# Optimization experiments

Hardware: AMD Instinct MI355X
Metric: run time of the kernel (lower is better)

## Reference

```python
import jax, jax.numpy as jnp
import numpy as np

H = 512   # hidden_size
E = 512   # embedding_size
V = 32000 # vocabulary_size
B = 64    # batch
TS = 256  # source length
TD = 64   # decoder (target) length


def setup_inputs() -> dict:
    key = jax.random.key(0)
    ks = jax.random.split(key, 10)
    s = lambda k, shape, sc: (jax.random.normal(k, shape, jnp.float32) * sc)
    return dict(
        src_seq=jax.random.randint(ks[0], (B, TS), 0, V, dtype=jnp.int32),
        dec_seq=jax.random.randint(ks[1], (B, TD), 0, V, dtype=jnp.int32),
        emb=s(ks[2], (V, E), 0.02),
        enc_Wx=s(ks[3], (E, 3 * H), 1.0 / np.sqrt(E)),
        enc_Wh=s(ks[4], (H, 3 * H), 1.0 / np.sqrt(H)),
        enc_b=jnp.zeros((3 * H,), jnp.float32),
        dec_Wx=s(ks[5], (E + H, 3 * H), 1.0 / np.sqrt(E + H)),
        dec_Wh=s(ks[6], (H, 3 * H), 1.0 / np.sqrt(H)),
        dec_b=jnp.zeros((3 * H,), jnp.float32),
        W_att=s(ks[7], (H, H), 1.0 / np.sqrt(H)),
        Wd=s(ks[8], (H, V), 1.0 / np.sqrt(H)),
        bd=jnp.zeros((V,), jnp.float32),
    )


def gru_step(h, x, Wx, Wh, b):
    # Keras GRUCell math (gate order z, r, h; reset_after applied on recurrent term)
    gx = x @ Wx + b            # [B, 3H]
    rec = h @ Wh               # [B, 3H]
    z = jax.nn.sigmoid(gx[:, :H] + rec[:, :H])
    r = jax.nn.sigmoid(gx[:, H:2 * H] + rec[:, H:2 * H])
    hh = jnp.tanh(gx[:, 2 * H:] + r * rec[:, 2 * H:])
    return z * h + (1.0 - z) * hh


def reference(src_seq, dec_seq, emb, enc_Wx, enc_Wh, enc_b,
              dec_Wx, dec_Wh, dec_b, W_att, Wd, bd):
    src_e = emb[src_seq]   # [B, TS, E]
    dec_e = emb[dec_seq]   # [B, TD, E]

    # ---- encoder: GRU over source, collecting hidden state each step ----
    def enc_f(h, x):
        h2 = gru_step(h, x, enc_Wx, enc_Wh, enc_b)
        return h2, h2

    h0 = jnp.zeros((src_e.shape[0], H), src_e.dtype)
    h_last, enc_hs = jax.lax.scan(enc_f, h0, jnp.swapaxes(src_e, 0, 1))
    enc_hs = jnp.swapaxes(enc_hs, 0, 1)  # [B, TS, H]

    # ---- decoder: Luong 'general' attention + GRU step each timestep ----
    def dec_f(h, x):
        q = h @ W_att                                          # [B, H]
        attn = jax.nn.softmax(jnp.einsum('bth,bh->bt', enc_hs, q), axis=-1)
        ctx = jnp.einsum('bt,bth->bh', attn, enc_hs)           # [B, H]
        inp = jnp.concatenate([x, ctx], axis=1)                # [B, E+H]
        h2 = gru_step(h, inp, dec_Wx, dec_Wh, dec_b)
        return h2, h2

    _, outs = jax.lax.scan(dec_f, h_last, jnp.swapaxes(dec_e, 0, 1))
    outs = jnp.swapaxes(outs, 0, 1)  # [B, TD, H]

    # ---- vocab projection ----
    logits = outs @ Wd + bd          # [B, TD, V]
    return logits
```

## Files before the change

kernel.cpp:

```cpp
#include <hip/hip_runtime.h>
#include <stdint.h>
#include <math.h>

#define B_   64
#define TS_  256
#define TD_  64
#define H_   512
#define E_   512
#define V_   32000
#define G3_  1536

#define ENC_G 0
#define ENC_T 128
#define ENC_F 160
#define DH_G  192
#define DH_T  320
#define DH_F  352
#define DP_G  384
#define DP_T  512
#define DP_F  544

typedef unsigned short u16;
typedef __attribute__((ext_vector_type(8))) short  short8v;
typedef __attribute__((ext_vector_type(4))) float  float4v;

__device__ __forceinline__ u16 f2bf(float x) {
  union { float f; unsigned u; } v; v.f = x;
  unsigned r = v.u + 0x7FFFu + ((v.u >> 16) & 1u);
  return (u16)(r >> 16);
}
__device__ __forceinline__ float bf2f(u16 h) {
  union { unsigned u; float f; } v; v.u = ((unsigned)h) << 16; return v.f;
}
__device__ __forceinline__ float sigm(float x) { return 1.f / (1.f + expf(-x)); }

__device__ __forceinline__ float4v mfma16(short8v a, short8v b, float4v c) {
  return __builtin_amdgcn_mfma_f32_16x16x32_bf16(a, b, c, 0, 0, 0);
}

__device__ __forceinline__ void st2_sc(u16* p, u16 v) {
  unsigned vv = v;
  asm volatile("global_store_short %0, %1, off sc0 sc1" :: "v"(p), "v"(vv) : "memory");
}
__device__ __forceinline__ void st4_sc(float* p, float v) {
  asm volatile("global_store_dword %0, %1, off sc0 sc1" :: "v"(p), "v"(v) : "memory");
}
__device__ __forceinline__ void st4u_sc(unsigned* p, unsigned v) {
  asm volatile("global_store_dword %0, %1, off sc0 sc1" :: "v"(p), "v"(v) : "memory");
}
__device__ __forceinline__ void st8_sc(float* p, float2 v) {
  asm volatile("global_store_dwordx2 %0, %1, off sc0 sc1" :: "v"(p), "v"(v) : "memory");
}
__device__ __forceinline__ short8v ld16_sc(const u16* p) {
  short8v r;
  asm volatile("global_load_dwordx4 %0, %1, off sc0 sc1\ns_waitcnt vmcnt(0)"
               : "=v"(r) : "v"(p) : "memory");
  return r;
}
__device__ __forceinline__ unsigned ld_cnt(const unsigned* p) {
  unsigned r;
  asm volatile("global_load_dword %0, %1, off sc0 sc1\ns_waitcnt vmcnt(0)"
               : "=v"(r) : "v"(p) : "memory");
  return r;
}

__device__ __forceinline__ void block_arrive(unsigned* bars, int goff, int grp,
                                             int toff, int foff, unsigned ngrp, unsigned step) {
  asm volatile("s_waitcnt vmcnt(0)" ::: "memory");
  __syncthreads();
  if (threadIdx.x == 0) {
    unsigned o = __hip_atomic_fetch_add(bars + goff + (grp << 5), 1u,
                                        __ATOMIC_RELAXED, __HIP_MEMORY_SCOPE_AGENT);
    if (o == step * 32u - 1u) {
      unsigned o2 = __hip_atomic_fetch_add(bars + toff, 1u,
                                           __ATOMIC_RELAXED, __HIP_MEMORY_SCOPE_AGENT);
      if (o2 == step * ngrp - 1u)
        st4u_sc(bars + foff, step);
    }
  }
}
__device__ __forceinline__ void wait_flag(unsigned* bars, int foff, unsigned step, unsigned* sdead) {
  __syncthreads();
  if (threadIdx.x == 0 && !*sdead) {
    unsigned spins = 0;
    while (ld_cnt(bars + foff) < step) {
      __builtin_amdgcn_s_sleep(4);
      if (++spins > (1u << 23)) { *sdead = 1u; break; }
    }
  }
  __syncthreads();
}

__global__ __launch_bounds__(256) void k_embed(const int* __restrict__ seq,
    const float* __restrict__ emb, u16* __restrict__ hi, u16* __restrict__ lo, int total8) {
  int idx = blockIdx.x * 256 + threadIdx.x;
  if (idx >= total8) return;
  int row = idx >> 6;
  int c8  = (idx & 63) << 3;
  const float* src = emb + (size_t)seq[row] * E_ + c8;
  short8v hv, lv;
  #pragma unroll
  for (int i = 0; i < 8; ++i) {
    float x = src[i];
    u16 hb2 = f2bf(x);
    hv[i] = (short)hb2;
    lv[i] = (short)f2bf(x - bf2f(hb2));
  }
  *(short8v*)(hi + (size_t)idx * 8) = hv;
  *(short8v*)(lo + (size_t)idx * 8) = lv;
}

template<bool LO>
__global__ __launch_bounds__(256) void k_transp(const float* __restrict__ src, int ld,
    u16* __restrict__ dh, u16* __restrict__ dl, int K, int N) {
  __shared__ float t[64][65];
  int n0 = blockIdx.x << 6, k0 = blockIdx.y << 6;
  int c = threadIdx.x & 63, r0 = threadIdx.x >> 6;
  #pragma unroll
  for (int i = 0; i < 16; ++i) {
    int r = r0 + (i << 2);
    t[r][c] = src[(size_t)(k0 + r) * ld + n0 + c];
  }
  __syncthreads();
  #pragma unroll
  for (int i = 0; i < 16; ++i) {
    int rr = r0 + (i << 2);
    float v = t[c][rr];
    u16 hb2 = f2bf(v);
    size_t o = (size_t)(n0 + rr) * K + k0 + c;
    dh[o] = hb2;
    if (LO) dl[o] = f2bf(v - bf2f(hb2));
  }
}

__global__ __launch_bounds__(256) void k_cvt(const float* __restrict__ s, u16* __restrict__ d, int n) {
  int i = blockIdx.x * 256 + threadIdx.x;
  if (i < n) d[i] = f2bf(s[i]);
}

__device__ __forceinline__ int swzA(int row, int q) {
  return (row << 5) + ((q ^ ((row >> 1) & 3)) << 3);
}

template<bool SPLIT, bool BF32N, bool BIAS, bool OBF>
__global__ __launch_bounds__(256, 2) void k_gemm(
    const u16* __restrict__ Ah, const u16* __restrict__ Al,
    const u16* __restrict__ Bh, const u16* __restrict__ Bl,
    const float* __restrict__ Bf,
    float* __restrict__ C, u16* __restrict__ Cb, const float* __restrict__ bias,
    int M, int N, int K)
{
  __shared__ u16 sA[4096], sB[4096];
  __shared__ u16 sA2[SPLIT ? 4096 : 16], sB2[SPLIT ? 4096 : 16];
  const int tid = threadIdx.x;
  const int ln = tid & 63, wv = tid >> 6;
  const int wr = wv >> 1, wc = wv & 1;
  const int m0 = blockIdx.y << 7, n0 = blockIdx.x << 7;
  const int lm = ln & 15, lq = ln >> 4;
  const float4v zf = {0.f, 0.f, 0.f, 0.f};

  float4v acc[4][4];
  #pragma unroll
  for (int i = 0; i < 4; ++i)
    #pragma unroll
    for (int j = 0; j < 4; ++j) acc[i][j] = zf;

  for (int kt = 0; kt < K; kt += 32) {
    #pragma unroll
    for (int s = 0; s < 2; ++s) {
      int id = tid + (s << 8);
      int row = id >> 2, q = id & 3;
      size_t goA = (size_t)(m0 + row) * K + kt + (q << 3);
      int lo = swzA(row, q);
      *(short8v*)&sA[lo] = *(const short8v*)(Ah + goA);
      if constexpr (!BF32N) {
        size_t goB = (size_t)(n0 + row) * K + kt + (q << 3);
        *(short8v*)&sB[lo] = *(const short8v*)(Bh + goB);
        if constexpr (SPLIT) {
          *(short8v*)&sA2[lo] = *(const short8v*)(Al + goA);
          *(short8v*)&sB2[lo] = *(const short8v*)(Bl + goB);
        }
      }
    }
    if constexpr (BF32N) {
      int k = tid >> 3, nc = (tid & 7) << 4;
      const float* bp = Bf + (size_t)(kt + k) * N + n0 + nc;
      int q = k >> 3, e = k & 7;
      #pragma unroll
      for (int j = 0; j < 16; ++j)
        sB[swzA(nc + j, q) + e] = f2bf(bp[j]);
    }
    __syncthreads();
    short8v af[4], bfr[4];
    #pragma unroll
    for (int i = 0; i < 4; ++i) {
      af[i]  = *(const short8v*)&sA[swzA((wr << 6) + (i << 4) + lm, lq)];
      bfr[i] = *(const short8v*)&sB[swzA((wc << 6) + (i << 4) + lm, lq)];
    }
    if constexpr (SPLIT) {
      short8v af2[4], bfr2[4];
      #pragma unroll
      for (int i = 0; i < 4; ++i) {
        af2[i]  = *(const short8v*)&sA2[swzA((wr << 6) + (i << 4) + lm, lq)];
        bfr2[i] = *(const short8v*)&sB2[swzA((wc << 6) + (i << 4) + lm, lq)];
      }
      #pragma unroll
      for (int mi = 0; mi < 4; ++mi)
        #pragma unroll
        for (int ni = 0; ni < 4; ++ni) {
          acc[mi][ni] = mfma16(af[mi],  bfr[ni],  acc[mi][ni]);
          acc[mi][ni] = mfma16(af2[mi], bfr[ni],  acc[mi][ni]);
          acc[mi][ni] = mfma16(af[mi],  bfr2[ni], acc[mi][ni]);
        }
    } else {
      #pragma unroll
      for (int mi = 0; mi < 4; ++mi)
        #pragma unroll
        for (int ni = 0; ni < 4; ++ni)
          acc[mi][ni] = mfma16(af[mi], bfr[ni], acc[mi][ni]);
    }
    __syncthreads();
  }
  #pragma unroll
  for (int mi = 0; mi < 4; ++mi)
    #pragma unroll
    for (int ni = 0; ni < 4; ++ni) {
      int col = n0 + (wc << 6) + (ni << 4) + lm;
      float bv = BIAS ? bias[col] : 0.f;
      #pragma unroll
      for (int i = 0; i < 4; ++i) {
        int row = m0 + (wr << 6) + (mi << 4) + (lq << 2) + i;
        float v = acc[mi][ni][i] + bv;
        size_t o = (size_t)row * N + col;
        if (OBF) Cb[o] = f2bf(v);
        else     C[o] = v;
      }
    }
}

__global__ __launch_bounds__(256, 1) void k_encoder(
    const float* __restrict__ gx, const float* __restrict__ Wh,
    u16* hb, u16* __restrict__ ehs, unsigned* bars)
{
  __shared__ char smem[32768];
  __shared__ float rec_s[3][16][16];
  __shared__ unsigned sdead;
  const int tid = threadIdx.x, bid = blockIdx.x;
  const int ln = tid & 63, wv = tid >> 6;
  const int lm = ln & 15, lq = ln >> 4, lq8 = lq << 3;
  const int set = bid >> 5, colblk = bid & 31, grp = bid >> 5;
  const int s16 = set << 4;
  const int jx = tid & 15, bl = tid >> 4;
  const int jg = (colblk << 4) + jx;
  const int b  = s16 + bl;
  if (tid == 0) sdead = 0;

  short8v wfh[16], wfl[16];
  if (wv < 3) {
    const int col = (wv << 9) + (colblk << 4) + lm;
    #pragma unroll
    for (int kt = 0; kt < 16; ++kt) {
      short8v a, b2;
      #pragma unroll
      for (int i = 0; i < 8; ++i) {
        float w = Wh[(size_t)((kt << 5) + lq8 + i) * G3_ + col];
        u16 hb2 = f2bf(w);
        a[i]  = (short)hb2;
        b2[i] = (short)f2bf(w - bf2f(hb2));
      }
      wfh[kt] = a; wfl[kt] = b2;
    }
  }
  const float4v zf = {0.f, 0.f, 0.f, 0.f};
  for (int t = 0; t < TS_; ++t) {
    if (t == 0) {
      short8v zz = {0,0,0,0,0,0,0,0};
      #pragma unroll
      for (int i = 0; i < 8; ++i)
        *(short8v*)(smem + ((tid + (i << 8)) << 4)) = zz;
      __syncthreads();
    } else {
      wait_flag(bars, ENC_F, (unsigned)t, &sdead);
      const u16* cur = hb + ((t & 1) ? 65536 : 0);
      short8v v[8];
      #pragma unroll
      for (int i = 0; i < 8; ++i) {
        int c = tid + (i << 8);
        int half = c >> 10, rem = c & 1023;
        int r = rem >> 6, col16 = rem & 63;
        const u16* p = cur + (half << 15) + ((s16 + r) << 9) + (col16 << 3);
        asm volatile("global_load_dwordx4 %0, %1, off sc0 sc1" : "=v"(v[i]) : "v"(p));
      }
      asm volatile("s_waitcnt vmcnt(0)" ::: "memory");
      __builtin_amdgcn_sched_barrier(0);
      #pragma unroll
      for (int i = 0; i < 8; ++i) {
        int c = tid + (i << 8);
        int half = c >> 10, rem = c & 1023;
        int r = rem >> 6, col16 = rem & 63;
        *(short8v*)(smem + ((half << 14) | (r << 10) | ((col16 << 4) ^ ((r & 7) << 4)))) = v[i];
      }
      __syncthreads();
    }
    float gzv, grv, ghv;
    {
      size_t rg = (size_t)((b << 8) + t) * G3_ + jg;
      gzv = gx[rg]; grv = gx[rg + 512]; ghv = gx[rg + 1024];
    }
    int hoff = (bl << 10) | ((jg << 1) ^ ((bl & 7) << 4));
    float hold = bf2f(*(const u16*)(smem + hoff)) + bf2f(*(const u16*)(smem + 16384 + hoff));
    if (wv < 3) {
      float4v acc = zf;
      #pragma unroll
      for (int kt = 0; kt < 16; ++kt) {
        int aoff = (lm << 10) | (((kt << 6) + (lq << 4)) ^ ((lm & 7) << 4));
        short8v ah = *(const short8v*)(smem + aoff);
        short8v al = *(const short8v*)(smem + 16384 + aoff);
        acc = mfma16(ah, wfh[kt], acc);
        acc = mfma16(al, wfh[kt], acc);
        acc = mfma16(ah, wfl[kt], acc);
      }
      #pragma unroll
      for (int i = 0; i < 4; ++i) rec_s[wv][(lq << 2) + i][lm] = acc[i];
    }
    __syncthreads();
    {
      float z  = sigm(gzv + rec_s[0][bl][jx]);
      float r  = sigm(grv + rec_s[1][bl][jx]);
      float hh = tanhf(ghv + r * rec_s[2][bl][jx]);
      float hnew = z * hold + (1.f - z) * hh;
      u16 nh = f2bf(hnew);
      u16* hnx = hb + ((t & 1) ? 0 : 65536);
      st2_sc(hnx + (b << 9) + jg, nh);
      st2_sc(hnx + 32768 + (b << 9) + jg, f2bf(hnew - bf2f(nh)));
      ehs[(size_t)((b << 8) + t) * 512 + jg] = nh;
    }
    if (t < TS_ - 1)
      block_arrive(bars, ENC_G, grp, ENC_T, ENC_F, 4u, (unsigned)(t + 1));
  }
}

__global__ __launch_bounds__(256, 1) void k_decoder(
    const float* __restrict__ gxd, const float* __restrict__ Wh,
    const u16* __restrict__ att, const u16* __restrict__ e2,
    u16* hb, float* pnum, float* pden, u16* __restrict__ outs, unsigned* bars)
{
  __shared__ char smem[32768];
  __shared__ float rec_s[3][16][16];
  __shared__ u16 shs[2][512];
  __shared__ float ps[128][2];
  __shared__ float es[128];
  __shared__ float wsum[2];
  __shared__ unsigned sdead;
  const int tid = threadIdx.x, bid = blockIdx.x;
  const int ln = tid & 63, wv = tid >> 6;
  const int lm = ln & 15, lq = ln >> 4, lq8 = lq << 3;
  const bool isrec = (bid < 128);
  const int set = bid >> 5, colblk = bid & 31;
  const int s16 = set << 4;
  const int jx = tid & 15, bl = tid >> 4;
  const int jg = (colblk << 4) + jx;
  const int b  = s16 + bl;
  const int ab = bid - 128, batt = ab >> 1, cset = ab & 1;
  if (tid == 0) sdead = 0;
  __syncthreads();

  short8v wfh[16], wfl[16];
  if (isrec && wv < 3) {
    const int col = (wv << 9) + (colblk << 4) + lm;
    #pragma unroll
    for (int kt = 0; kt < 16; ++kt) {
      short8v a, b2;
      #pragma unroll
      for (int i = 0; i < 8; ++i) {
        float w = Wh[(size_t)((kt << 5) + lq8 + i) * G3_ + col];
        u16 hb2 = f2bf(w);
        a[i]  = (short)hb2;
        b2[i] = (short)f2bf(w - bf2f(hb2));
      }
      wfh[kt] = a; wfl[kt] = b2;
    }
  }
  const float4v zf = {0.f, 0.f, 0.f, 0.f};
  for (int t = 0; t < TD_; ++t) {
    const u16* cur = hb + ((t & 1) ? 65536 : 0);
    if (isrec) {
      if (t) wait_flag(bars, DH_F, (unsigned)t, &sdead);
      {
        short8v v[8];
        #pragma unroll
        for (int i = 0; i < 8; ++i) {
          int c = tid + (i << 8);
          int half = c >> 10, rem = c & 1023;
          int r = rem >> 6, col16 = rem & 63;
          const u16* p = cur + (half << 15) + ((s16 + r) << 9) + (col16 << 3);
          asm volatile("global_load_dwordx4 %0, %1, off sc0 sc1" : "=v"(v[i]) : "v"(p));
        }
        asm volatile("s_waitcnt vmcnt(0)" ::: "memory");
        __builtin_amdgcn_sched_barrier(0);
        #pragma unroll
        for (int i = 0; i < 8; ++i) {
          int c = tid + (i << 8);
          int half = c >> 10, rem = c & 1023;
          int r = rem >> 6, col16 = rem & 63;
          *(short8v*)(smem + ((half << 14) | (r << 10) | ((col16 << 4) ^ ((r & 7) << 4)))) = v[i];
        }
        __syncthreads();
      }
      float gzv, grv, ghv;
      {
        size_t rg = (size_t)((b << 6) + t) * G3_ + jg;
        gzv = gxd[rg]; grv = gxd[rg + 512]; ghv = gxd[rg + 1024];
      }
      int hoff = (bl << 10) | ((jg << 1) ^ ((bl & 7) << 4));
      float hold = bf2f(*(const u16*)(smem + hoff)) + bf2f(*(const u16*)(smem + 16384 + hoff));
      if (wv < 3) {
        float4v acc = zf;
        #pragma unroll
        for (int kt = 0; kt < 16; ++kt) {
          int aoff = (lm << 10) | (((kt << 6) + (lq << 4)) ^ ((lm & 7) << 4));
          short8v ah = *(const short8v*)(smem + aoff);
          short8v al = *(const short8v*)(smem + 16384 + aoff);
          acc = mfma16(ah, wfh[kt], acc);
          acc = mfma16(al, wfh[kt], acc);
          acc = mfma16(ah, wfl[kt], acc);
        }
        #pragma unroll
        for (int i = 0; i < 4; ++i) rec_s[wv][(lq << 2) + i][lm] = acc[i];
      }
      __syncthreads();
      wait_flag(bars, DP_F, (unsigned)(t + 1), &sdead);
      {
        const float* p0 = pnum + (size_t)(b << 1) * G3_ + jg;
        const float* p1 = p0 + G3_;
        float pv0, pv1, pv2, pv3, pv4, pv5, d0, d1;
        asm volatile("global_load_dword %0, %1, off sc0 sc1" : "=v"(pv0) : "v"(p0));
        asm volatile("global_load_dword %0, %1, off sc0 sc1" : "=v"(pv1) : "v"(p0 + 512));
        asm volatile("global_load_dword %0, %1, off sc0 sc1" : "=v"(pv2) : "v"(p0 + 1024));
        asm volatile("global_load_dword %0, %1, off sc0 sc1" : "=v"(pv3) : "v"(p1));
        asm volatile("global_load_dword %0, %1, off sc0 sc1" : "=v"(pv4) : "v"(p1 + 512));
        asm volatile("global_load_dword %0, %1, off sc0 sc1" : "=v"(pv5) : "v"(p1 + 1024));
        asm volatile("global_load_dword %0, %1, off sc0 sc1" : "=v"(d0) : "v"(pden + (b << 1)));
        asm volatile("global_load_dword %0, %1, off sc0 sc1" : "=v"(d1) : "v"(pden + (b << 1) + 1));
        asm volatile("s_waitcnt vmcnt(0)" ::: "memory");
        __builtin_amdgcn_sched_barrier(0);
        float inv = 1.f / (d0 + d1);
        float z  = sigm(gzv + (pv0 + pv3) * inv + rec_s[0][bl][jx]);
        float r  = sigm(grv + (pv1 + pv4) * inv + rec_s[1][bl][jx]);
        float hh = tanhf(ghv + (pv2 + pv5) * inv + r * rec_s[2][bl][jx]);
        float hnew = z * hold + (1.f - z) * hh;
        u16 nh = f2bf(hnew);
        outs[(size_t)((b << 6) + t) * 512 + jg] = nh;
        if (t < TD_ - 1) {
          u16* hnx = hb + ((t & 1) ? 0 : 65536);
          st2_sc(hnx + (b << 9) + jg, nh);
          st2_sc(hnx + 32768 + (b << 9) + jg, f2bf(hnew - bf2f(nh)));
        }
      }
      if (t < TD_ - 1)
        block_arrive(bars, DH_G, set, DH_T, DH_F, 4u, (unsigned)(t + 1));
    } else {
      if (t) wait_flag(bars, DH_F, (unsigned)t, &sdead);
      if (tid < 128) {
        int half = tid >> 6, cc = tid & 63;
        short8v hv = ld16_sc(cur + (half << 15) + (batt << 9) + (cc << 3));
        *(short8v*)&shs[half][cc << 3] = hv;
      }
      __syncthreads();
      {
        int tt = tid >> 1, kq = tid & 1;
        const u16* ep = att + (size_t)((batt << 8) + (cset << 7) + tt) * 512 + (kq << 8);
        float s = 0.f;
        #pragma unroll 4
        for (int k8 = 0; k8 < 32; ++k8) {
          short8v ev = *(const short8v*)(ep + (k8 << 3));
          short8v xh = *(const short8v*)&shs[0][(kq << 8) + (k8 << 3)];
          short8v xl = *(const short8v*)&shs[1][(kq << 8) + (k8 << 3)];
          #pragma unroll
          for (int i = 0; i < 8; ++i)
            s += bf2f((u16)ev[i]) * (bf2f((u16)xh[i]) + bf2f((u16)xl[i]));
        }
        ps[tt][kq] = s;
      }
      __syncthreads();
      if (tid < 128) {
        float e = expf(ps[tid][0] + ps[tid][1]);
        es[tid] = e;
        #pragma unroll
        for (int off = 32; off; off >>= 1) e += __shfl_down(e, off);
        if ((tid & 63) == 0) wsum[tid >> 6] = e;
      }
      __syncthreads();
      if (tid == 0) st4_sc(&pden[(batt << 1) + cset], wsum[0] + wsum[1]);
      {
        int c0 = tid * 6;
        float a0=0.f,a1=0.f,a2=0.f,a3=0.f,a4=0.f,a5=0.f;
        const u16* base = e2 + (size_t)((batt << 8) + (cset << 7)) * G3_ + c0;
        for (int tt = 0; tt < 128; ++tt) {
          float ev = es[tt];
          const u16* p = base + (size_t)tt * G3_;
          a0 += ev * bf2f(p[0]); a1 += ev * bf2f(p[1]); a2 += ev * bf2f(p[2]);
          a3 += ev * bf2f(p[3]); a4 += ev * bf2f(p[4]); a5 += ev * bf2f(p[5]);
        }
        float* pn = pnum + (size_t)((batt << 1) + cset) * G3_ + c0;
        float2 v01 = {a0, a1}, v23 = {a2, a3}, v45 = {a4, a5};
        st8_sc(pn, v01); st8_sc(pn + 2, v23); st8_sc(pn + 4, v45);
      }
      block_arrive(bars, DP_G, ab >> 5, DP_T, DP_F, 4u, (unsigned)(t + 1));
    }
  }
}

extern "C" void kernel_launch(void* const* d_in, const int* in_sizes, int n_in,
                              void* d_out, int out_size, void* d_ws, size_t ws_size,
                              hipStream_t stream) {
  const int*   src_seq = (const int*)d_in[0];
  const int*   dec_seq = (const int*)d_in[1];
  const float* emb     = (const float*)d_in[2];
  const float* enc_Wx  = (const float*)d_in[3];
  const float* enc_Wh  = (const float*)d_in[4];
  const float* enc_b   = (const float*)d_in[5];
  const float* dec_Wx  = (const float*)d_in[6];
  const float* dec_Wh  = (const float*)d_in[7];
  const float* dec_b   = (const float*)d_in[8];
  const float* W_att   = (const float*)d_in[9];
  const float* Wd      = (const float*)d_in[10];
  const float* bd      = (const float*)d_in[11];

  char* ob = (char*)d_out;
  float* gx_all  = (float*)(ob + 0);
  float* gxd_all = (float*)(ob + 100663296);
  u16* srcE_h = (u16*)(ob + 125829120);
  u16* srcE_l = (u16*)(ob + 142606336);
  u16* decE_h = (u16*)(ob + 159383552);
  u16* decE_l = (u16*)(ob + 163577856);
  u16* ehs    = (u16*)(ob + 167772160);
  u16* attb   = (u16*)(ob + 184549376);
  u16* e2b    = (u16*)(ob + 201326592);
  u16* wxT_h  = (u16*)(ob + 251658240);
  u16* wxT_l  = (u16*)(ob + 253231104);
  u16* wdxT_h = (u16*)(ob + 254803968);
  u16* wdxT_l = (u16*)(ob + 256376832);
  u16* wxcT   = (u16*)(ob + 257949696);
  u16* watt   = (u16*)(ob + 259522560);
  u16* hbuf   = (u16*)(ob + 260046848);

  char* wb = (char*)d_ws;
  u16* outs     = (u16*)(wb + 0);
  float* pnum   = (float*)(wb + 4194304);
  float* pden   = (float*)(wb + 4980736);
  unsigned* bars = (unsigned*)(wb + 4981248);
  (void)in_sizes; (void)n_in; (void)out_size; (void)ws_size;

  hipMemsetAsync(bars, 0, 4096, stream);

  k_embed<<<4096, 256, 0, stream>>>(src_seq, emb, srcE_h, srcE_l, B_*TS_*64);
  k_embed<<<1024, 256, 0, stream>>>(dec_seq, emb, decE_h, decE_l, B_*TD_*64);
  k_transp<true ><<<dim3(24, 8), 256, 0, stream>>>(enc_Wx, G3_, wxT_h,  wxT_l,  512, G3_);
  k_transp<true ><<<dim3(24, 8), 256, 0, stream>>>(dec_Wx, G3_, wdxT_h, wdxT_l, 512, G3_);
  k_transp<false><<<dim3(24, 8), 256, 0, stream>>>(dec_Wx + (size_t)512*G3_, G3_, wxcT, nullptr, 512, G3_);
  k_cvt<<<1024, 256, 0, stream>>>(W_att, watt, 512*512);

  k_gemm<true, false, true, false><<<dim3(12, 128), 256, 0, stream>>>(
      srcE_h, srcE_l, wxT_h, wxT_l, nullptr, gx_all, nullptr, enc_b, 16384, G3_, 512);
  k_gemm<true, false, true, false><<<dim3(12, 32), 256, 0, stream>>>(
      decE_h, decE_l, wdxT_h, wdxT_l, nullptr, gxd_all, nullptr, dec_b, 4096, G3_, 512);

  k_encoder<<<128, 256, 0, stream>>>(gx_all, enc_Wh, hbuf, ehs, bars);

  k_gemm<false, false, false, true><<<dim3(4, 128), 256, 0, stream>>>(
      ehs, nullptr, watt, nullptr, nullptr, nullptr, attb, nullptr, 16384, 512, 512);
  k_gemm<false, false, false, true><<<dim3(12, 128), 256, 0, stream>>>(
      ehs, nullptr, wxcT, nullptr, nullptr, nullptr, e2b, nullptr, 16384, G3_, 512);

  k_decoder<<<256, 256, 0, stream>>>(gxd_all, dec_Wh, attb, e2b, hbuf, pnum, pden, outs, bars);

  k_gemm<false, true, true, false><<<dim3(250, 32), 256, 0, stream>>>(
      outs, nullptr, nullptr, nullptr, Wd, (float*)d_out, nullptr, bd, 4096, V_, 512);
}
```

Before: 3.128 ms.

## Replace global atomic barriers with per-set flag slots and vectorize attention loops

Swaps the two-level atomic counter barrier for per-block step slots. Each block writes its own slot and waiters poll all 32 slots of their 16-batch set with a wavefront vote, so the wait is local to dependent blocks instead of grid-wide. The attention blocks also precombine the hi/lo hidden state into fp32 in shared memory, and they register-prefetch 16-byte vector loads in both the score and context-weighted e2 loops. The e2 loop is split across four waves with a shared-memory reduction. This adds polling traffic (32 loads per wait) and more shared memory and registers.

```diff
diff --git a/kernel.cpp b/kernel.cpp
--- a/kernel.cpp
+++ b/kernel.cpp
@@ -10,15 +10,9 @@
 #define V_   32000
 #define G3_  1536
 
-#define ENC_G 0
-#define ENC_T 128
-#define ENC_F 160
-#define DH_G  192
-#define DH_T  320
-#define DH_F  352
-#define DP_G  384
-#define DP_T  512
-#define DP_F  544
+#define ENC_S 0
+#define DH_S  256
+#define DP_S  512
 
 typedef unsigned short u16;
 typedef __attribute__((ext_vector_type(8))) short  short8v;
@@ -64,28 +58,21 @@
   return r;
 }
 
-__device__ __forceinline__ void block_arrive(unsigned* bars, int goff, int grp,
-                                             int toff, int foff, unsigned ngrp, unsigned step) {
+__device__ __forceinline__ void arrive_slot(unsigned* slot, unsigned step) {
   asm volatile("s_waitcnt vmcnt(0)" ::: "memory");
   __syncthreads();
-  if (threadIdx.x == 0) {
-    unsigned o = __hip_atomic_fetch_add(bars + goff + (grp << 5), 1u,
-                                        __ATOMIC_RELAXED, __HIP_MEMORY_SCOPE_AGENT);
-    if (o == step * 32u - 1u) {
-      unsigned o2 = __hip_atomic_fetch_add(bars + toff, 1u,
-                                           __ATOMIC_RELAXED, __HIP_MEMORY_SCOPE_AGENT);
-      if (o2 == step * ngrp - 1u)
-        st4u_sc(bars + foff, step);
-    }
-  }
-}
-__device__ __forceinline__ void wait_flag(unsigned* bars, int foff, unsigned step, unsigned* sdead) {
+  if (threadIdx.x == 0) st4u_sc(slot, step);
+}
+__device__ __forceinline__ void wait_slots(const unsigned* slots, unsigned step, unsigned* sdead) {
   __syncthreads();
-  if (threadIdx.x == 0 && !*sdead) {
+  if (threadIdx.x < 64 && !*sdead) {
     unsigned spins = 0;
-    while (ld_cnt(bars + foff) < step) {
-      __builtin_amdgcn_s_sleep(4);
-      if (++spins > (1u << 23)) { *sdead = 1u; break; }
+    for (;;) {
+      unsigned v = step;
+      if (threadIdx.x < 32) v = ld_cnt(slots + threadIdx.x);
+      if (__all(v >= step)) break;
+      __builtin_amdgcn_s_sleep(2);
+      if (++spins > (1u << 22)) { if (threadIdx.x == 0) *sdead = 1u; break; }
     }
   }
   __syncthreads();
@@ -248,11 +235,12 @@
   const int tid = threadIdx.x, bid = blockIdx.x;
   const int ln = tid & 63, wv = tid >> 6;
   const int lm = ln & 15, lq = ln >> 4, lq8 = lq << 3;
-  const int set = bid >> 5, colblk = bid & 31, grp = bid >> 5;
+  const int set = bid >> 5, colblk = bid & 31;
   const int s16 = set << 4;
   const int jx = tid & 15, bl = tid >> 4;
   const int jg = (colblk << 4) + jx;
   const int b  = s16 + bl;
+  unsigned* slots = bars + ENC_S + (set << 5);
   if (tid == 0) sdead = 0;
 
   short8v wfh[16], wfl[16];
@@ -280,7 +268,7 @@
         *(short8v*)(smem + ((tid + (i << 8)) << 4)) = zz;
       __syncthreads();
     } else {
-      wait_flag(bars, ENC_F, (unsigned)t, &sdead);
+      wait_slots(slots, (unsigned)t, &sdead);
       const u16* cur = hb + ((t & 1) ? 65536 : 0);
       short8v v[8];
       #pragma unroll
@@ -336,7 +324,7 @@
       ehs[(size_t)((b << 8) + t) * 512 + jg] = nh;
     }
     if (t < TS_ - 1)
-      block_arrive(bars, ENC_G, grp, ENC_T, ENC_F, 4u, (unsigned)(t + 1));
+      arrive_slot(slots + colblk, (unsigned)(t + 1));
   }
 }
 
@@ -347,9 +335,10 @@
 {
   __shared__ char smem[32768];
   __shared__ float rec_s[3][16][16];
-  __shared__ u16 shs[2][512];
+  __shared__ float hsumf[512];
   __shared__ float ps[128][2];
   __shared__ float es[128];
+  __shared__ float psum[4][64][24];
   __shared__ float wsum[2];
   __shared__ unsigned sdead;
   const int tid = threadIdx.x, bid = blockIdx.x;
@@ -361,7 +350,7 @@
   const int jx = tid & 15, bl = tid >> 4;
   const int jg = (colblk << 4) + jx;
   const int b  = s16 + bl;
-  const int ab = bid - 128, batt = ab >> 1, cset = ab & 1;
+  const int ab = bid - 128, batt = ab >> 1, cset = ab & 1, sb = (ab >> 1) >> 4;
   if (tid == 0) sdead = 0;
   __syncthreads();
 
@@ -385,7 +374,9 @@
   for (int t = 0; t < TD_; ++t) {
     const u16* cur = hb + ((t & 1) ? 65536 : 0);
     if (isrec) {
-      if (t) wait_flag(bars, DH_F, (unsigned)t, &sdead);
+      unsigned* dhs = bars + DH_S + (set << 5);
+      unsigned* dps = bars + DP_S + (set << 5);
+      if (t) wait_slots(dhs, (unsigned)t, &sdead);
       {
         short8v v[8];
         #pragma unroll
@@ -428,8 +419,7 @@
         #pragma unroll
         for (int i = 0; i < 4; ++i) rec_s[wv][(lq << 2) + i][lm] = acc[i];
       }
-      __syncthreads();
-      wait_flag(bars, DP_F, (unsigned)(t + 1), &sdead);
+      wait_slots(dps, (unsigned)(t + 1), &sdead);
       {
         const float* p0 = pnum + (size_t)(b << 1) * G3_ + jg;
         const float* p1 = p0 + G3_;
@@ -458,27 +448,37 @@
         }
       }
       if (t < TD_ - 1)
-        block_arrive(bars, DH_G, set, DH_T, DH_F, 4u, (unsigned)(t + 1));
+        arrive_slot(dhs + colblk, (unsigned)(t + 1));
     } else {
-      if (t) wait_flag(bars, DH_F, (unsigned)t, &sdead);
-      if (tid < 128) {
-        int half = tid >> 6, cc = tid & 63;
-        short8v hv = ld16_sc(cur + (half << 15) + (batt << 9) + (cc << 3));
-        *(short8v*)&shs[half][cc << 3] = hv;
+      unsigned* dhs = bars + DH_S + (sb << 5);
+      unsigned* dps = bars + DP_S + (sb << 5);
+      if (t) wait_slots(dhs, (unsigned)t, &sdead);
+      if (tid < 64) {
+        short8v hv = ld16_sc(cur + (batt << 9) + (tid << 3));
+        short8v lv = ld16_sc(cur + 32768 + (batt << 9) + (tid << 3));
+        #pragma unroll
+        for (int j = 0; j < 8; ++j)
+          hsumf[(tid << 3) + j] = bf2f((u16)hv[j]) + bf2f((u16)lv[j]);
       }
       __syncthreads();
       {
         int tt = tid >> 1, kq = tid & 1;
         const u16* ep = att + (size_t)((batt << 8) + (cset << 7) + tt) * 512 + (kq << 8);
+        short8v q[8];
+        #pragma unroll
+        for (int i = 0; i < 8; ++i) q[i] = *(const short8v*)(ep + (i << 3));
         float s = 0.f;
-        #pragma unroll 4
-        for (int k8 = 0; k8 < 32; ++k8) {
-          short8v ev = *(const short8v*)(ep + (k8 << 3));
-          short8v xh = *(const short8v*)&shs[0][(kq << 8) + (k8 << 3)];
-          short8v xl = *(const short8v*)&shs[1][(kq << 8) + (k8 << 3)];
+        #pragma unroll
+        for (int g = 0; g < 4; ++g) {
           #pragma unroll
-          for (int i = 0; i < 8; ++i)
-            s += bf2f((u16)ev[i]) * (bf2f((u16)xh[i]) + bf2f((u16)xl[i]));
+          for (int i = 0; i < 8; ++i) {
+            short8v curq = q[i];
+            if (g < 3) q[i] = *(const short8v*)(ep + ((((g + 1) << 3) + i) << 3));
+            const int kb = (kq << 8) + (((g << 3) + i) << 3);
+            #pragma unroll
+            for (int j = 0; j < 8; ++j)
+              s += bf2f((u16)curq[j]) * hsumf[kb + j];
+          }
         }
         ps[tt][kq] = s;
       }
@@ -493,20 +493,55 @@
       __syncthreads();
       if (tid == 0) st4_sc(&pden[(batt << 1) + cset], wsum[0] + wsum[1]);
       {
-        int c0 = tid * 6;
-        float a0=0.f,a1=0.f,a2=0.f,a3=0.f,a4=0.f,a5=0.f;
-        const u16* base = e2 + (size_t)((batt << 8) + (cset << 7)) * G3_ + c0;
-        for (int tt = 0; tt < 128; ++tt) {
-          float ev = es[tt];
-          const u16* p = base + (size_t)tt * G3_;
-          a0 += ev * bf2f(p[0]); a1 += ev * bf2f(p[1]); a2 += ev * bf2f(p[2]);
-          a3 += ev * bf2f(p[3]); a4 += ev * bf2f(p[4]); a5 += ev * bf2f(p[5]);
-        }
-        float* pn = pnum + (size_t)((batt << 1) + cset) * G3_ + c0;
-        float2 v01 = {a0, a1}, v23 = {a2, a3}, v45 = {a4, a5};
+        int qt = tid >> 6, cg = tid & 63;
+        const u16* base = e2 + (size_t)((batt << 8) + (cset << 7) + (qt << 5)) * G3_ + cg * 24;
+        short8v q0[4], q1[4], q2[4];
+        #pragma unroll
+        for (int i = 0; i < 4; ++i) {
+          const u16* p = base + (size_t)i * G3_;
+          q0[i] = *(const short8v*)(p);
+          q1[i] = *(const short8v*)(p + 8);
+          q2[i] = *(const short8v*)(p + 16);
+        }
+        float a[24];
+        #pragma unroll
+        for (int j = 0; j < 24; ++j) a[j] = 0.f;
+        #pragma unroll
+        for (int g = 0; g < 8; ++g) {
+          #pragma unroll
+          for (int i = 0; i < 4; ++i) {
+            short8v c0 = q0[i], c1 = q1[i], c2 = q2[i];
+            if (g < 7) {
+              const u16* nb = base + (size_t)(((g + 1) << 2) + i) * G3_;
+              q0[i] = *(const short8v*)(nb);
+              q1[i] = *(const short8v*)(nb + 8);
+              q2[i] = *(const short8v*)(nb + 16);
+            }
+            float w = es[(qt << 5) + (g << 2) + i];
+            #pragma unroll
+            for (int j = 0; j < 8; ++j) {
+              a[j]      += w * bf2f((u16)c0[j]);
+              a[8 + j]  += w * bf2f((u16)c1[j]);
+              a[16 + j] += w * bf2f((u16)c2[j]);
+            }
+          }
+        }
+        #pragma unroll
+        for (int j = 0; j < 24; ++j) psum[qt][cg][j] = a[j];
+      }
+      __syncthreads();
+      {
+        int rcg = tid >> 2, ro = (tid & 3) * 6;
+        float r[6];
+        #pragma unroll
+        for (int j = 0; j < 6; ++j)
+          r[j] = psum[0][rcg][ro + j] + psum[1][rcg][ro + j]
+               + psum[2][rcg][ro + j] + psum[3][rcg][ro + j];
+        float* pn = pnum + (size_t)((batt << 1) + cset) * G3_ + tid * 6;
+        float2 v01 = {r[0], r[1]}, v23 = {r[2], r[3]}, v45 = {r[4], r[5]};
         st8_sc(pn, v01); st8_sc(pn + 2, v23); st8_sc(pn + 4, v45);
       }
-      block_arrive(bars, DP_G, ab >> 5, DP_T, DP_F, 4u, (unsigned)(t + 1));
+      arrive_slot(dps + (ab & 31), (unsigned)(t + 1));
     }
   }
 }
```

Result: slower. 3.657 ms (+16.9%).

## Compute attention query per step instead of precomputing ehs·W_att GEMM

Applied to the files above, without the earlier changes.

The score is reassociated from (enc_hs·W_att)·h to enc_hs·(W_att·h). This drops the separate 16384x512x512 GEMM that produced the attention keys, and each attention block now computes its query q = W_att·h inside the decoder step from a transposed bf16 W_att. The context accumulation is also widened to 8-column vectorized loads with 16-byte stores. The cost is extra per-step serial work in the decoder's critical path, since every attention block recomputes a 512x512 matvec, and precision changes slightly because ehs is now used directly.

```diff
diff --git a/kernel.cpp b/kernel.cpp
--- a/kernel.cpp
+++ b/kernel.cpp
@@ -48,8 +48,8 @@
 __device__ __forceinline__ void st4u_sc(unsigned* p, unsigned v) {
   asm volatile("global_store_dword %0, %1, off sc0 sc1" :: "v"(p), "v"(v) : "memory");
 }
-__device__ __forceinline__ void st8_sc(float* p, float2 v) {
-  asm volatile("global_store_dwordx2 %0, %1, off sc0 sc1" :: "v"(p), "v"(v) : "memory");
+__device__ __forceinline__ void st16f_sc(float* p, float4v v) {
+  asm volatile("global_store_dwordx4 %0, %1, off sc0 sc1" :: "v"(p), "v"(v) : "memory");
 }
 __device__ __forceinline__ short8v ld16_sc(const u16* p) {
   short8v r;
@@ -131,11 +131,6 @@
     dh[o] = hb2;
     if (LO) dl[o] = f2bf(v - bf2f(hb2));
   }
-}
-
-__global__ __launch_bounds__(256) void k_cvt(const float* __restrict__ s, u16* __restrict__ d, int n) {
-  int i = blockIdx.x * 256 + threadIdx.x;
-  if (i < n) d[i] = f2bf(s[i]);
 }
 
 __device__ __forceinline__ int swzA(int row, int q) {
@@ -342,12 +337,14 @@
 
 __global__ __launch_bounds__(256, 1) void k_decoder(
     const float* __restrict__ gxd, const float* __restrict__ Wh,
-    const u16* __restrict__ att, const u16* __restrict__ e2,
+    const u16* __restrict__ wattT, const u16* __restrict__ ehs, const u16* __restrict__ e2,
     u16* hb, float* pnum, float* pden, u16* __restrict__ outs, unsigned* bars)
 {
   __shared__ char smem[32768];
   __shared__ float rec_s[3][16][16];
-  __shared__ u16 shs[2][512];
+  __shared__ float hsumf[512];
+  __shared__ float qpart[2][512];
+  __shared__ float q_lds[512];
   __shared__ float ps[128][2];
   __shared__ float es[128];
   __shared__ float wsum[2];
@@ -461,24 +458,56 @@
         block_arrive(bars, DH_G, set, DH_T, DH_F, 4u, (unsigned)(t + 1));
     } else {
       if (t) wait_flag(bars, DH_F, (unsigned)t, &sdead);
+      if (tid < 64) {
+        short8v hv = ld16_sc(cur + (batt << 9) + (tid << 3));
+        short8v lv = ld16_sc(cur + 32768 + (batt << 9) + (tid << 3));
+        #pragma unroll
+        for (int j = 0; j < 8; ++j)
+          hsumf[(tid << 3) + j] = bf2f((u16)hv[j]) + bf2f((u16)lv[j]);
+      }
+      __syncthreads();
+      {
+        int cq = (tid & 127) << 2;
+        int kh = tid >> 7;
+        const u16* w0 = wattT + (size_t)cq * 512 + (kh << 8);
+        float a0 = 0.f, a1 = 0.f, a2 = 0.f, a3 = 0.f;
+        #pragma unroll 4
+        for (int kc = 0; kc < 32; ++kc) {
+          short8v r0 = *(const short8v*)(w0 + (kc << 3));
+          short8v r1 = *(const short8v*)(w0 + 512 + (kc << 3));
+          short8v r2 = *(const short8v*)(w0 + 1024 + (kc << 3));
+          short8v r3 = *(const short8v*)(w0 + 1536 + (kc << 3));
+          #pragma unroll
+          for (int j = 0; j < 8; ++j) {
+            float hv = hsumf[(kh << 8) + (kc << 3) + j];
+            a0 += hv * bf2f((u16)r0[j]);
+            a1 += hv * bf2f((u16)r1[j]);
+            a2 += hv * bf2f((u16)r2[j]);
+            a3 += hv * bf2f((u16)r3[j]);
+          }
+        }
+        qpart[kh][cq] = a0; qpart[kh][cq + 1] = a1;
+        qpart[kh][cq + 2] = a2; qpart[kh][cq + 3] = a3;
+      }
+      __syncthreads();
       if (tid < 128) {
-        int half = tid >> 6, cc = tid & 63;
-        short8v hv = ld16_sc(cur + (half << 15) + (batt << 9) + (cc << 3));
-        *(short8v*)&shs[half][cc << 3] = hv;
+        #pragma unroll
+        for (int j = 0; j < 4; ++j) {
+          int c = (tid << 2) + j;
+          q_lds[c] = qpart[0][c] + qpart[1][c];
+        }
       }
       __syncthreads();
       {
         int tt = tid >> 1, kq = tid & 1;
-        const u16* ep = att + (size_t)((batt << 8) + (cset << 7) + tt) * 512 + (kq << 8);
+        const u16* ep = ehs + (size_t)((batt << 8) + (cset << 7) + tt) * 512 + (kq << 8);
         float s = 0.f;
         #pragma unroll 4
         for (int k8 = 0; k8 < 32; ++k8) {
           short8v ev = *(const short8v*)(ep + (k8 << 3));
-          short8v xh = *(const short8v*)&shs[0][(kq << 8) + (k8 << 3)];
-          short8v xl = *(const short8v*)&shs[1][(kq << 8) + (k8 << 3)];
           #pragma unroll
           for (int i = 0; i < 8; ++i)
-            s += bf2f((u16)ev[i]) * (bf2f((u16)xh[i]) + bf2f((u16)xl[i]));
+            s += bf2f((u16)ev[i]) * q_lds[(kq << 8) + (k8 << 3) + i];
         }
         ps[tt][kq] = s;
       }
@@ -492,19 +521,23 @@
       }
       __syncthreads();
       if (tid == 0) st4_sc(&pden[(batt << 1) + cset], wsum[0] + wsum[1]);
-      {
-        int c0 = tid * 6;
-        float a0=0.f,a1=0.f,a2=0.f,a3=0.f,a4=0.f,a5=0.f;
+      if (tid < 192) {
+        int c0 = tid << 3;
         const u16* base = e2 + (size_t)((batt << 8) + (cset << 7)) * G3_ + c0;
-        for (int tt = 0; tt < 128; ++tt) {
-          float ev = es[tt];
-          const u16* p = base + (size_t)tt * G3_;
-          a0 += ev * bf2f(p[0]); a1 += ev * bf2f(p[1]); a2 += ev * bf2f(p[2]);
-          a3 += ev * bf2f(p[3]); a4 += ev * bf2f(p[4]); a5 += ev * bf2f(p[5]);
+        float a[8] = {0.f,0.f,0.f,0.f,0.f,0.f,0.f,0.f};
+        #pragma unroll 4
+        for (int tt2 = 0; tt2 < 128; ++tt2) {
+          short8v cv = *(const short8v*)(base + (size_t)tt2 * G3_);
+          float w = es[tt2];
+          #pragma unroll
+          for (int j = 0; j < 8; ++j)
+            a[j] += w * bf2f((u16)cv[j]);
         }
         float* pn = pnum + (size_t)((batt << 1) + cset) * G3_ + c0;
-        float2 v01 = {a0, a1}, v23 = {a2, a3}, v45 = {a4, a5};
-        st8_sc(pn, v01); st8_sc(pn + 2, v23); st8_sc(pn + 4, v45);
+        float4v v0 = {a[0], a[1], a[2], a[3]};
+        float4v v1 = {a[4], a[5], a[6], a[7]};
+        st16f_sc(pn, v0);
+        st16f_sc(pn + 4, v1);
       }
       block_arrive(bars, DP_G, ab >> 5, DP_T, DP_F, 4u, (unsigned)(t + 1));
     }
@@ -535,14 +568,13 @@
   u16* decE_h = (u16*)(ob + 159383552);
   u16* decE_l = (u16*)(ob + 163577856);
   u16* ehs    = (u16*)(ob + 167772160);
-  u16* attb   = (u16*)(ob + 184549376);
   u16* e2b    = (u16*)(ob + 201326592);
   u16* wxT_h  = (u16*)(ob + 251658240);
   u16* wxT_l  = (u16*)(ob + 253231104);
   u16* wdxT_h = (u16*)(ob + 254803968);
   u16* wdxT_l = (u16*)(ob + 256376832);
   u16* wxcT   = (u16*)(ob + 257949696);
-  u16* watt   = (u16*)(ob + 259522560);
+  u16* wattT  = (u16*)(ob + 259522560);
   u16* hbuf   = (u16*)(ob + 260046848);
 
   char* wb = (char*)d_ws;
@@ -559,7 +591,7 @@
   k_transp<true ><<<dim3(24, 8), 256, 0, stream>>>(enc_Wx, G3_, wxT_h,  wxT_l,  512, G3_);
   k_transp<true ><<<dim3(24, 8), 256, 0, stream>>>(dec_Wx, G3_, wdxT_h, wdxT_l, 512, G3_);
   k_transp<false><<<dim3(24, 8), 256, 0, stream>>>(dec_Wx + (size_t)512*G3_, G3_, wxcT, nullptr, 512, G3_);
-  k_cvt<<<1024, 256, 0, stream>>>(W_att, watt, 512*512);
+  k_transp<false><<<dim3(8, 8),  256, 0, stream>>>(W_att, 512, wattT, nullptr, 512, 512);
 
   k_gemm<true, false, true, false><<<dim3(12, 128), 256, 0, stream>>>(
       srcE_h, srcE_l, wxT_h, wxT_l, nullptr, gx_all, nullptr, enc_b, 16384, G3_, 512);
@@ -568,12 +600,11 @@
 
   k_encoder<<<128, 256, 0, stream>>>(gx_all, enc_Wh, hbuf, ehs, bars);
 
-  k_gemm<false, false, false, true><<<dim3(4, 128), 256, 0, stream>>>(
-      ehs, nullptr, watt, nullptr, nullptr, nullptr, attb, nullptr, 16384, 512, 512);
   k_gemm<false, false, false, true><<<dim3(12, 128), 256, 0, stream>>>(
       ehs, nullptr, wxcT, nullptr, nullptr, nullptr, e2b, nullptr, 16384, G3_, 512);
 
-  k_decoder<<<256, 256, 0, stream>>>(gxd_all, dec_Wh, attb, e2b, hbuf, pnum, pden, outs, bars);
+  k_decoder<<<256, 256, 0, stream>>>(gxd_all, dec_Wh, wattT, ehs, e2b,
+                                     hbuf, pnum, pden, outs, bars);
 
   k_gemm<false, true, true, false><<<dim3(250, 32), 256, 0, stream>>>(
       outs, nullptr, nullptr, nullptr, Wd, (float*)d_out, nullptr, bd, 4096, V_, 512);
```

Result: slower. 6.249 ms (+99.8%).
